# Optimization experiments

Hardware: AMD Instinct MI355X
Metric: run time of the kernel (lower is better)

The kernel has to match this reference:

```python
import jax, jax.numpy as jnp
import numpy as np

CLAMP = 1.0e6
LN_EPS = 1e-5
TWO_PI = 6.283185307179586


def _layernorm_last(x, gamma, beta):
    mu = jnp.mean(x, axis=-1, keepdims=True)
    var = jnp.var(x, axis=-1, keepdims=True)
    return (x - mu) * jax.lax.rsqrt(var + LN_EPS) * gamma + beta


def _candidates(xc):
    # xc: (C, B, S, D) pre-scaled + clamped input, one slice per candidate
    return jnp.stack([
        xc[0],
        xc[1] * xc[1],
        jnp.cos(TWO_PI * xc[2]),
        jnp.sin(xc[3]),
        jnp.exp(xc[4]),
        jnp.ones_like(xc[5]),
        xc[6] * xc[6] * xc[6],
        jnp.log(jnp.abs(xc[7]) + 1.0),
        jnp.sqrt(jnp.abs(xc[8])),
        jnp.tanh(xc[9]),
    ], axis=0)


def setup_inputs() -> dict:
    key = jax.random.key(0)
    ks = jax.random.split(key, 5)
    B, S, D, C = 4, 2048, 1024, 10
    return {
        "x": jax.random.normal(ks[0], (B, S, D), dtype=jnp.float32),
        "ln_gamma": jnp.ones((D,), dtype=jnp.float32),
        "ln_beta": jnp.zeros((D,), dtype=jnp.float32),
        "log_in_scale": jax.random.normal(ks[1], (C,), dtype=jnp.float32) * 0.05,
        "log_out_scale": jax.random.normal(ks[2], (C,), dtype=jnp.float32) * 0.05,
        "gate_w": jax.random.normal(ks[3], (C, D), dtype=jnp.float32) * (D ** -0.5),
        "gate_b": jnp.zeros((C,), dtype=jnp.float32),
    }


def reference(x, ln_gamma, ln_beta, log_in_scale, log_out_scale, gate_w, gate_b):
    # Input LayerNorm over D
    x_norm = _layernorm_last(x, ln_gamma, ln_beta)  # (B,S,D)

    in_s = jnp.exp(log_in_scale)    # (C,)
    out_s = jnp.exp(log_out_scale)  # (C,)

    # Per-candidate input scale + clamp
    xc = x_norm[None] * in_s[:, None, None, None]          # (C,B,S,D)
    xc = jnp.clip(xc, -CLAMP, CLAMP)

    cand = _candidates(xc) * out_s[:, None, None, None]    # (C,B,S,D)
    cand = jnp.clip(cand, -CLAMP, CLAMP)

    # permute to (B,S,C,D) and LayerNorm jointly over (C,D), no affine
    cand = jnp.transpose(cand, (1, 2, 0, 3))                # (B,S,C,D)
    mu = jnp.mean(cand, axis=(2, 3), keepdims=True)
    var = jnp.var(cand, axis=(2, 3), keepdims=True)
    cand = (cand - mu) * jax.lax.rsqrt(var + LN_EPS)
    cand = jnp.clip(cand, -CLAMP, CLAMP)
    cand = jnp.nan_to_num(cand, nan=0.0, posinf=CLAMP, neginf=-CLAMP)

    # Gate on the RAW input x (as in the torch code), softmax over candidates
    gate_logits = jnp.einsum('bsd,cd->bsc', x, gate_w) + gate_b  # (B,S,C)
    gate_weights = jax.nn.softmax(gate_logits, axis=-1)

    # Weighted sum over the candidate axis
    weighted = jnp.einsum('bsc,bscd->bsd', gate_weights, cand)   # (B,S,D)
    return weighted, gate_weights
```

## Files before the change

kernel.cpp:

```cpp
#include <hip/hip_runtime.h>
#include <math.h>

constexpr int D_DIM = 1024;
constexpr int C_DIM = 10;
constexpr int WPB   = 8;
constexpr int BLOCK = 64 * WPB;

constexpr float CLAMP_V  = 1.0e6f;
constexpr float LOG2E    = 1.4426950408889634f;
constexpr float LN2      = 0.6931471805599453f;
constexpr float INV_2PI  = 0.15915494309189535f;

__device__ __forceinline__ float2 pmul(float2 a, float2 b) {
    return make_float2(a.x * b.x, a.y * b.y);
}
__device__ __forceinline__ float2 pfma(float2 a, float2 b, float2 c) {
    return make_float2(fmaf(a.x, b.x, c.x), fmaf(a.y, b.y, c.y));
}
__device__ __forceinline__ float2 padd(float2 a, float2 b) {
    return make_float2(a.x + b.x, a.y + b.y);
}
__device__ __forceinline__ float2 bc(float s) { return make_float2(s, s); }

__device__ __forceinline__ float rfl(float x) {
    return __int_as_float(__builtin_amdgcn_readfirstlane(__float_as_int(x)));
}

template <int CTRL>
__device__ __forceinline__ float dpp_add(float v) {
    const int s = __builtin_amdgcn_update_dpp(
        0, __float_as_int(v), CTRL, 0xf, 0xf, false);
    return v + __int_as_float(s);
}
__device__ __forceinline__ float wave_sum_sgpr(float v) {
    v = dpp_add<0x111>(v);
    v = dpp_add<0x112>(v);
    v = dpp_add<0x114>(v);
    v = dpp_add<0x118>(v);
    v = dpp_add<0x142>(v);
    v = dpp_add<0x143>(v);
    return __int_as_float(__builtin_amdgcn_readlane(__float_as_int(v), 63));
}

__global__ __launch_bounds__(BLOCK)
void fused_sme_kernel(const float* __restrict__ x,
                      const float* __restrict__ ln_gamma,
                      const float* __restrict__ ln_beta,
                      const float* __restrict__ log_in_scale,
                      const float* __restrict__ log_out_scale,
                      const float* __restrict__ gate_w,
                      const float* __restrict__ gate_b,
                      float* __restrict__ out_weighted,
                      float* __restrict__ out_gate,
                      int tokens)
{
    const int t    = threadIdx.x;
    const int lane = t & 63;
    int token = blockIdx.x * WPB + (t >> 6);
    token = min(token, tokens - 1);

    __shared__ float gws[C_DIM * D_DIM];

    const float* xrow = x + (size_t)token * D_DIM;
    float4 xv[4];
#pragma unroll
    for (int k = 0; k < 4; ++k)
        xv[k] = *reinterpret_cast<const float4*>(xrow + k * 256 + (lane << 2));

#pragma unroll
    for (int i = 0; i < 5; ++i) {
        const int idx = t + i * BLOCK;
        reinterpret_cast<float4*>(gws)[idx] =
            reinterpret_cast<const float4*>(gate_w)[idx];
    }

    float r[12];
    {
        float2 s = bc(0.0f), q = bc(0.0f);
#pragma unroll
        for (int k = 0; k < 4; ++k) {
            const float2 lo = make_float2(xv[k].x, xv[k].y);
            const float2 hi = make_float2(xv[k].z, xv[k].w);
            s = padd(s, padd(lo, hi));
            q = pfma(lo, lo, q);
            q = pfma(hi, hi, q);
        }
        r[0] = wave_sum_sgpr(s.x + s.y);
        r[1] = wave_sum_sgpr(q.x + q.y);
    }

    __syncthreads();

#pragma unroll
    for (int c = 0; c < C_DIM; ++c) {
        const float* gr = gws + c * D_DIM + (lane << 2);
        float2 d2 = bc(0.0f);
#pragma unroll
        for (int k = 0; k < 4; ++k) {
            const float4 gw = *reinterpret_cast<const float4*>(gr + k * 256);
            d2 = pfma(make_float2(xv[k].x, xv[k].y), make_float2(gw.x, gw.y), d2);
            d2 = pfma(make_float2(xv[k].z, xv[k].w), make_float2(gw.z, gw.w), d2);
        }
        r[2 + c] = wave_sum_sgpr(d2.x + d2.y);
    }

    const float mu   = r[0] * (1.0f / D_DIM);
    const float var  = r[1] * (1.0f / D_DIM) - mu * mu;
    const float rstd = rfl(rsqrtf(var + 1e-5f));

    float w[C_DIM];
    float gmax = -3.4e38f;
#pragma unroll
    for (int c = 0; c < C_DIM; ++c) {
        w[c] = r[2 + c] + gate_b[c];
        gmax = fmaxf(gmax, w[c]);
    }
    float esum = 0.0f;
#pragma unroll
    for (int c = 0; c < C_DIM; ++c) {
        w[c] = __builtin_amdgcn_exp2f((w[c] - gmax) * LOG2E);
        esum += w[c];
    }
    const float rsum = __builtin_amdgcn_rcpf(esum);
#pragma unroll
    for (int c = 0; c < C_DIM; ++c) w[c] = rfl(w[c] * rsum);

    if (lane < C_DIM) out_gate[token * C_DIM + lane] = w[lane];

    float in_s[C_DIM], out_s[C_DIM];
#pragma unroll
    for (int c = 0; c < C_DIM; ++c) {
        in_s[c]  = __builtin_amdgcn_exp2f(log_in_scale[c]  * LOG2E);
        out_s[c] = __builtin_amdgcn_exp2f(log_out_scale[c] * LOG2E);
    }
    const float a0 = rfl(out_s[0] * in_s[0]);
    const float a1 = rfl(out_s[1] * in_s[1] * in_s[1]);
    const float k2 = rfl(in_s[2]),           o2 = rfl(out_s[2]);
    const float k3 = rfl(in_s[3] * INV_2PI), o3 = rfl(out_s[3]);
    const float k4 = rfl(in_s[4] * LOG2E),   o4 = rfl(out_s[4]);
    const float v5 = rfl(fminf(out_s[5], CLAMP_V));
    const float a6 = rfl(out_s[6] * in_s[6] * in_s[6] * in_s[6]);
    const float k7 = rfl(in_s[7]),           o7 = rfl(out_s[7] * LN2);
    const float k8 = rfl(in_s[8]),           o8 = rfl(out_s[8]);
    const float k9 = rfl(2.0f * in_s[9] * LOG2E);
    const float o9 = rfl(out_s[9]),          m9 = rfl(-2.0f * out_s[9]);

    float2 xn[8];
#pragma unroll
    for (int k = 0; k < 4; ++k) {
        const float4 gv = *reinterpret_cast<const float4*>(ln_gamma + k * 256 + (lane << 2));
        const float4 bv = *reinterpret_cast<const float4*>(ln_beta  + k * 256 + (lane << 2));
        const float2 zlo = pmul(padd(make_float2(xv[k].x, xv[k].y), bc(-mu)), bc(rstd));
        const float2 zhi = pmul(padd(make_float2(xv[k].z, xv[k].w), bc(-mu)), bc(rstd));
        xn[2 * k]     = pfma(zlo, make_float2(gv.x, gv.y), make_float2(bv.x, bv.y));
        xn[2 * k + 1] = pfma(zhi, make_float2(gv.z, gv.w), make_float2(bv.z, bv.w));
    }

    const float accbase = rfl(w[5] * v5);
    float2 S1 = bc(0.0f), S2 = bc(0.0f);

#pragma unroll
    for (int p = 0; p < 8; ++p) {
        const float2 xj = xn[p];
        const float2 ax = make_float2(fabsf(xj.x), fabsf(xj.y));
        const float2 x2 = pmul(xj, xj);

        const float2 v0 = pmul(bc(a0), xj);
        const float2 v1 = pmul(bc(a1), x2);

        float2 u2 = pmul(bc(k2), xj);
        u2 = padd(u2, make_float2(-rintf(u2.x), -rintf(u2.y)));
        const float2 v2 = pmul(bc(o2),
            make_float2(__builtin_amdgcn_cosf(u2.x), __builtin_amdgcn_cosf(u2.y)));

        float2 u3 = pmul(bc(k3), xj);
        u3 = padd(u3, make_float2(-rintf(u3.x), -rintf(u3.y)));
        const float2 v3 = pmul(bc(o3),
            make_float2(__builtin_amdgcn_sinf(u3.x), __builtin_amdgcn_sinf(u3.y)));

        const float2 u4 = pmul(bc(k4), xj);
        float2 v4 = pmul(bc(o4),
            make_float2(__builtin_amdgcn_exp2f(u4.x), __builtin_amdgcn_exp2f(u4.y)));
        v4 = make_float2(fminf(v4.x, CLAMP_V), fminf(v4.y, CLAMP_V));

        const float2 v6 = pmul(bc(a6), pmul(x2, xj));

        const float2 u7 = pfma(bc(k7), ax, bc(1.0f));
        const float2 v7 = pmul(bc(o7),
            make_float2(__builtin_amdgcn_logf(u7.x), __builtin_amdgcn_logf(u7.y)));

        const float2 u8 = pmul(bc(k8), ax);
        const float2 v8 = pmul(bc(o8),
            make_float2(__builtin_amdgcn_sqrtf(u8.x), __builtin_amdgcn_sqrtf(u8.y)));

        const float2 u9 = pmul(bc(k9), xj);
        const float2 e9 = padd(
            make_float2(__builtin_amdgcn_exp2f(u9.x), __builtin_amdgcn_exp2f(u9.y)),
            bc(1.0f));
        const float2 v9 = pfma(bc(m9),
            make_float2(__builtin_amdgcn_rcpf(e9.x), __builtin_amdgcn_rcpf(e9.y)),
            bc(o9));

        S1 = padd(S1, padd(padd(padd(v0, v1), padd(v2, v3)),
                           padd(padd(v4, v6), padd(padd(v7, v8), v9))));
        S2 = pfma(v0, v0, S2); S2 = pfma(v1, v1, S2); S2 = pfma(v2, v2, S2);
        S2 = pfma(v3, v3, S2); S2 = pfma(v4, v4, S2); S2 = pfma(v6, v6, S2);
        S2 = pfma(v7, v7, S2); S2 = pfma(v8, v8, S2); S2 = pfma(v9, v9, S2);

        float2 a = bc(accbase);
        a = pfma(bc(w[0]), v0, a); a = pfma(bc(w[1]), v1, a);
        a = pfma(bc(w[2]), v2, a); a = pfma(bc(w[3]), v3, a);
        a = pfma(bc(w[4]), v4, a); a = pfma(bc(w[6]), v6, a);
        a = pfma(bc(w[7]), v7, a); a = pfma(bc(w[8]), v8, a);
        a = pfma(bc(w[9]), v9, a);
        xn[p] = a;
    }

    const float s1 = wave_sum_sgpr(S1.x + S1.y + 16.0f * v5);
    const float s2 = wave_sum_sgpr(fmaf(16.0f * v5, v5, S2.x + S2.y));

    constexpr float rn = 1.0f / (float)(C_DIM * D_DIM);
    const float mu2  = s1 * rn;
    const float var2 = s2 * rn - mu2 * mu2;
    const float rsig = rfl(rsqrtf(var2 + 1e-5f));

    float* orow = out_weighted + (size_t)token * D_DIM;
#pragma unroll
    for (int k = 0; k < 4; ++k) {
        const float2 lo = pmul(padd(xn[2 * k],     bc(-mu2)), bc(rsig));
        const float2 hi = pmul(padd(xn[2 * k + 1], bc(-mu2)), bc(rsig));
        float4 o;
        o.x = lo.x; o.y = lo.y; o.z = hi.x; o.w = hi.y;
        *reinterpret_cast<float4*>(orow + k * 256 + (lane << 2)) = o;
    }
}

extern "C" void kernel_launch(void* const* d_in, const int* in_sizes, int n_in,
                              void* d_out, int out_size, void* d_ws, size_t ws_size,
                              hipStream_t stream) {
    const float* x   = (const float*)d_in[0];
    const float* lg  = (const float*)d_in[1];
    const float* lb  = (const float*)d_in[2];
    const float* lis = (const float*)d_in[3];
    const float* los = (const float*)d_in[4];
    const float* gw  = (const float*)d_in[5];
    const float* gb  = (const float*)d_in[6];

    const int tokens = in_sizes[0] / D_DIM;
    float* out      = (float*)d_out;
    float* out_gate = out + (size_t)tokens * D_DIM;

    const int grid = (tokens + WPB - 1) / WPB;
    hipLaunchKernelGGL(fused_sme_kernel, dim3(grid), dim3(BLOCK), 0, stream,
                       x, lg, lb, lis, los, gw, gb, out, out_gate, tokens);
}
```

Baseline: 29.76 us.

## Split each token across two waves and stage only nine gate rows in LDS

Each token is now handled by two wavefronts, each covering half of D, so a 512-thread block processes 4 tokens instead of 8. Partial sums for the LayerNorm statistics, gate logits and candidate statistics are combined through a small shared reduction array, which adds extra __syncthreads. Gate row 0 is read directly from global memory and only rows 1-9 are staged in LDS, making the LDS footprint smaller. The aim is more parallelism per token and less register pressure, at the cost of twice as many blocks, each of which reloads the gate weights, plus extra barriers.

```diff
diff --git a/kernel.cpp b/kernel.cpp
--- a/kernel.cpp
+++ b/kernel.cpp
@@ -3,8 +3,8 @@
 
 constexpr int D_DIM = 1024;
 constexpr int C_DIM = 10;
-constexpr int WPB   = 8;
-constexpr int BLOCK = 64 * WPB;
+constexpr int TPB   = 4;
+constexpr int BLOCK = 512;
 
 constexpr float CLAMP_V  = 1.0e6f;
 constexpr float LOG2E    = 1.4426950408889634f;
@@ -56,53 +56,75 @@
 {
     const int t    = threadIdx.x;
     const int lane = t & 63;
-    int token = blockIdx.x * WPB + (t >> 6);
+    const int h    = (t >> 6) & 1;
+    const int tl   = t >> 7;
+    int token = blockIdx.x * TPB + tl;
     token = min(token, tokens - 1);
 
-    __shared__ float gws[C_DIM * D_DIM];
-
-    const float* xrow = x + (size_t)token * D_DIM;
-    float4 xv[4];
-#pragma unroll
-    for (int k = 0; k < 4; ++k)
-        xv[k] = *reinterpret_cast<const float4*>(xrow + k * 256 + (lane << 2));
+    __shared__ float gws[9 * D_DIM];
+    __shared__ float red[TPB][2][14];
+
+    const int eoff = h * 512 + (lane << 2);
+    const float* xrow = x + (size_t)token * D_DIM + eoff;
+    float4 xv[2];
+#pragma unroll
+    for (int k = 0; k < 2; ++k)
+        xv[k] = *reinterpret_cast<const float4*>(xrow + k * 256);
 
 #pragma unroll
     for (int i = 0; i < 5; ++i) {
         const int idx = t + i * BLOCK;
-        reinterpret_cast<float4*>(gws)[idx] =
-            reinterpret_cast<const float4*>(gate_w)[idx];
+        if (idx < 9 * D_DIM / 4)
+            reinterpret_cast<float4*>(gws)[idx] =
+                reinterpret_cast<const float4*>(gate_w + D_DIM)[idx];
     }
 
     float r[12];
     {
-        float2 s = bc(0.0f), q = bc(0.0f);
-#pragma unroll
-        for (int k = 0; k < 4; ++k) {
+        float2 s = bc(0.0f), q = bc(0.0f), d0 = bc(0.0f);
+        const float* g0 = gate_w + eoff;
+#pragma unroll
+        for (int k = 0; k < 2; ++k) {
+            const float4 gv = *reinterpret_cast<const float4*>(g0 + k * 256);
             const float2 lo = make_float2(xv[k].x, xv[k].y);
             const float2 hi = make_float2(xv[k].z, xv[k].w);
             s = padd(s, padd(lo, hi));
             q = pfma(lo, lo, q);
             q = pfma(hi, hi, q);
+            d0 = pfma(lo, make_float2(gv.x, gv.y), d0);
+            d0 = pfma(hi, make_float2(gv.z, gv.w), d0);
         }
         r[0] = wave_sum_sgpr(s.x + s.y);
         r[1] = wave_sum_sgpr(q.x + q.y);
-    }
-
+        r[2] = wave_sum_sgpr(d0.x + d0.y);
+    }
+    if (lane == 0) {
+        red[tl][h][0] = r[0]; red[tl][h][1] = r[1]; red[tl][h][2] = r[2];
+    }
     __syncthreads();
-
-#pragma unroll
-    for (int c = 0; c < C_DIM; ++c) {
-        const float* gr = gws + c * D_DIM + (lane << 2);
+    r[0] += red[tl][h ^ 1][0];
+    r[1] += red[tl][h ^ 1][1];
+    r[2] += red[tl][h ^ 1][2];
+
+#pragma unroll
+    for (int c = 1; c < C_DIM; ++c) {
+        const float* gr = gws + (c - 1) * D_DIM + eoff;
         float2 d2 = bc(0.0f);
 #pragma unroll
-        for (int k = 0; k < 4; ++k) {
-            const float4 gw = *reinterpret_cast<const float4*>(gr + k * 256);
-            d2 = pfma(make_float2(xv[k].x, xv[k].y), make_float2(gw.x, gw.y), d2);
-            d2 = pfma(make_float2(xv[k].z, xv[k].w), make_float2(gw.z, gw.w), d2);
+        for (int k = 0; k < 2; ++k) {
+            const float4 gv = *reinterpret_cast<const float4*>(gr + k * 256);
+            d2 = pfma(make_float2(xv[k].x, xv[k].y), make_float2(gv.x, gv.y), d2);
+            d2 = pfma(make_float2(xv[k].z, xv[k].w), make_float2(gv.z, gv.w), d2);
         }
         r[2 + c] = wave_sum_sgpr(d2.x + d2.y);
     }
+    if (lane == 0) {
+#pragma unroll
+        for (int c = 1; c < C_DIM; ++c) red[tl][h][2 + c] = r[2 + c];
+    }
+    __syncthreads();
+#pragma unroll
+    for (int c = 1; c < C_DIM; ++c) r[2 + c] += red[tl][h ^ 1][2 + c];
 
     const float mu   = r[0] * (1.0f / D_DIM);
     const float var  = r[1] * (1.0f / D_DIM) - mu * mu;
@@ -125,7 +147,7 @@
 #pragma unroll
     for (int c = 0; c < C_DIM; ++c) w[c] = rfl(w[c] * rsum);
 
-    if (lane < C_DIM) out_gate[token * C_DIM + lane] = w[lane];
+    if (h == 0 && lane < C_DIM) out_gate[token * C_DIM + lane] = w[lane];
 
     float in_s[C_DIM], out_s[C_DIM];
 #pragma unroll
@@ -145,11 +167,11 @@
     const float k9 = rfl(2.0f * in_s[9] * LOG2E);
     const float o9 = rfl(out_s[9]),          m9 = rfl(-2.0f * out_s[9]);
 
-    float2 xn[8];
-#pragma unroll
-    for (int k = 0; k < 4; ++k) {
-        const float4 gv = *reinterpret_cast<const float4*>(ln_gamma + k * 256 + (lane << 2));
-        const float4 bv = *reinterpret_cast<const float4*>(ln_beta  + k * 256 + (lane << 2));
+    float2 xn[4];
+#pragma unroll
+    for (int k = 0; k < 2; ++k) {
+        const float4 gv = *reinterpret_cast<const float4*>(ln_gamma + eoff + k * 256);
+        const float4 bv = *reinterpret_cast<const float4*>(ln_beta  + eoff + k * 256);
         const float2 zlo = pmul(padd(make_float2(xv[k].x, xv[k].y), bc(-mu)), bc(rstd));
         const float2 zhi = pmul(padd(make_float2(xv[k].z, xv[k].w), bc(-mu)), bc(rstd));
         xn[2 * k]     = pfma(zlo, make_float2(gv.x, gv.y), make_float2(bv.x, bv.y));
@@ -160,7 +182,7 @@
     float2 S1 = bc(0.0f), S2 = bc(0.0f);
 
 #pragma unroll
-    for (int p = 0; p < 8; ++p) {
+    for (int p = 0; p < 4; ++p) {
         const float2 xj = xn[p];
         const float2 ax = make_float2(fabsf(xj.x), fabsf(xj.y));
         const float2 x2 = pmul(xj, xj);
@@ -216,22 +238,26 @@
         xn[p] = a;
     }
 
-    const float s1 = wave_sum_sgpr(S1.x + S1.y + 16.0f * v5);
-    const float s2 = wave_sum_sgpr(fmaf(16.0f * v5, v5, S2.x + S2.y));
+    float s1 = wave_sum_sgpr(S1.x + S1.y + 8.0f * v5);
+    float s2 = wave_sum_sgpr(fmaf(8.0f * v5, v5, S2.x + S2.y));
+    if (lane == 0) { red[tl][h][12] = s1; red[tl][h][13] = s2; }
+    __syncthreads();
+    s1 += red[tl][h ^ 1][12];
+    s2 += red[tl][h ^ 1][13];
 
     constexpr float rn = 1.0f / (float)(C_DIM * D_DIM);
     const float mu2  = s1 * rn;
     const float var2 = s2 * rn - mu2 * mu2;
     const float rsig = rfl(rsqrtf(var2 + 1e-5f));
 
-    float* orow = out_weighted + (size_t)token * D_DIM;
-#pragma unroll
-    for (int k = 0; k < 4; ++k) {
+    float* orow = out_weighted + (size_t)token * D_DIM + eoff;
+#pragma unroll
+    for (int k = 0; k < 2; ++k) {
         const float2 lo = pmul(padd(xn[2 * k],     bc(-mu2)), bc(rsig));
         const float2 hi = pmul(padd(xn[2 * k + 1], bc(-mu2)), bc(rsig));
         float4 o;
         o.x = lo.x; o.y = lo.y; o.z = hi.x; o.w = hi.y;
-        *reinterpret_cast<float4*>(orow + k * 256 + (lane << 2)) = o;
+        *reinterpret_cast<float4*>(orow + k * 256) = o;
     }
 }
 
@@ -250,7 +276,7 @@
     float* out      = (float*)d_out;
     float* out_gate = out + (size_t)tokens * D_DIM;
 
-    const int grid = (tokens + WPB - 1) / WPB;
+    const int grid = (tokens + TPB - 1) / TPB;
     hipLaunchKernelGGL(fused_sme_kernel, dim3(grid), dim3(BLOCK), 0, stream,
                        x, lg, lb, lis, los, gw, gb, out, out_gate, tokens);
 }
```

Measured after the change: 36.48 us. 1.23x slower.

## Split gate logits into separate MFMA kernel using split-bf16 emulation

Applied to the files above, without the earlier changes.

Moves the gate projection (x times gate_w) out of the fused kernel into its own kernel. That kernel computes 16-token tiles with bf16 MFMA instructions and uses a three-term hi/lo split to keep near-fp32 accuracy. The fused kernel then reads the logits from workspace, which drops the 40 KB shared-memory staging of gate_w per block and the ten per-token wave reductions. In exchange it adds a second launch, a second full read of x, and a workspace round-trip for the logits; block size also changes from 512 to 256 threads.

```diff
diff --git a/kernel.cpp b/kernel.cpp
--- a/kernel.cpp
+++ b/kernel.cpp
@@ -3,13 +3,14 @@
 
 constexpr int D_DIM = 1024;
 constexpr int C_DIM = 10;
-constexpr int WPB   = 8;
-constexpr int BLOCK = 64 * WPB;
 
 constexpr float CLAMP_V  = 1.0e6f;
 constexpr float LOG2E    = 1.4426950408889634f;
 constexpr float LN2      = 0.6931471805599453f;
 constexpr float INV_2PI  = 0.15915494309189535f;
+
+using bf16x8 = __attribute__((ext_vector_type(8))) short;
+using f32x4  = __attribute__((ext_vector_type(4))) float;
 
 __device__ __forceinline__ float2 pmul(float2 a, float2 b) {
     return make_float2(a.x * b.x, a.y * b.y);
@@ -42,77 +43,107 @@
     return __int_as_float(__builtin_amdgcn_readlane(__float_as_int(v), 63));
 }
 
-__global__ __launch_bounds__(BLOCK)
-void fused_sme_kernel(const float* __restrict__ x,
-                      const float* __restrict__ ln_gamma,
-                      const float* __restrict__ ln_beta,
-                      const float* __restrict__ log_in_scale,
-                      const float* __restrict__ log_out_scale,
-                      const float* __restrict__ gate_w,
-                      const float* __restrict__ gate_b,
-                      float* __restrict__ out_weighted,
-                      float* __restrict__ out_gate,
-                      int tokens)
+__global__ __launch_bounds__(64)
+void logits_kernel(const float* __restrict__ x,
+                   const float* __restrict__ gate_w,
+                   const float* __restrict__ gate_b,
+                   float* __restrict__ logits,
+                   int tokens)
 {
-    const int t    = threadIdx.x;
-    const int lane = t & 63;
-    int token = blockIdx.x * WPB + (t >> 6);
+    const int l    = threadIdx.x;
+    const int col  = l & 15;
+    const int kgrp = l >> 4;
+
+    const int tile = blockIdx.x;
+    const int arow = min(tile * 16 + col, tokens - 1);
+    const int wrow = (col < C_DIM) ? col : 0;
+    const float bm = (col < C_DIM) ? 1.0f : 0.0f;
+
+    const float* px = x + (size_t)arow * D_DIM + (kgrp << 3);
+    const float* pw = gate_w + (size_t)wrow * D_DIM + (kgrp << 3);
+
+    f32x4 acc0 = {0.f, 0.f, 0.f, 0.f};
+    f32x4 acc1 = {0.f, 0.f, 0.f, 0.f};
+    f32x4 acc2 = {0.f, 0.f, 0.f, 0.f};
+
+    for (int ks = 0; ks < D_DIM / 32; ++ks) {
+        const float4 a0 = *reinterpret_cast<const float4*>(px + ks * 32);
+        const float4 a1 = *reinterpret_cast<const float4*>(px + ks * 32 + 4);
+        const float4 b0 = *reinterpret_cast<const float4*>(pw + ks * 32);
+        const float4 b1 = *reinterpret_cast<const float4*>(pw + ks * 32 + 4);
+
+        const float af[8] = {a0.x, a0.y, a0.z, a0.w, a1.x, a1.y, a1.z, a1.w};
+        const float bf[8] = {b0.x * bm, b0.y * bm, b0.z * bm, b0.w * bm,
+                             b1.x * bm, b1.y * bm, b1.z * bm, b1.w * bm};
+        bf16x8 ah, al, bh, bl;
+#pragma unroll
+        for (int j = 0; j < 8; ++j) {
+            const unsigned ua = __float_as_uint(af[j]);
+            ah[j] = (short)(ua >> 16);
+            al[j] = (short)(__float_as_uint(
+                        af[j] - __uint_as_float(ua & 0xffff0000u)) >> 16);
+            const unsigned ub = __float_as_uint(bf[j]);
+            bh[j] = (short)(ub >> 16);
+            bl[j] = (short)(__float_as_uint(
+                        bf[j] - __uint_as_float(ub & 0xffff0000u)) >> 16);
+        }
+        acc0 = __builtin_amdgcn_mfma_f32_16x16x32_bf16(ah, bh, acc0, 0, 0, 0);
+        acc1 = __builtin_amdgcn_mfma_f32_16x16x32_bf16(ah, bl, acc1, 0, 0, 0);
+        acc2 = __builtin_amdgcn_mfma_f32_16x16x32_bf16(al, bh, acc2, 0, 0, 0);
+    }
+
+    const float bias = (col < C_DIM) ? gate_b[col] : 0.0f;
+#pragma unroll
+    for (int r = 0; r < 4; ++r) {
+        const int trow = tile * 16 + (l >> 4) * 4 + r;
+        if (trow < tokens)
+            logits[trow * 16 + col] = (acc0[r] + acc1[r]) + acc2[r] + bias;
+    }
+}
+
+__global__ __launch_bounds__(256)
+void fused_kernel(const float* __restrict__ x,
+                  const float* __restrict__ ln_gamma,
+                  const float* __restrict__ ln_beta,
+                  const float* __restrict__ log_in_scale,
+                  const float* __restrict__ log_out_scale,
+                  const float* __restrict__ logits,
+                  float* __restrict__ out_weighted,
+                  float* __restrict__ out_gate,
+                  int tokens)
+{
+    const int lane = threadIdx.x & 63;
+    int token = blockIdx.x * 4 + (threadIdx.x >> 6);
     token = min(token, tokens - 1);
 
-    __shared__ float gws[C_DIM * D_DIM];
-
-    const float* xrow = x + (size_t)token * D_DIM;
+    const float* xrow = x + (size_t)token * D_DIM + (lane << 2);
     float4 xv[4];
 #pragma unroll
     for (int k = 0; k < 4; ++k)
-        xv[k] = *reinterpret_cast<const float4*>(xrow + k * 256 + (lane << 2));
-
-#pragma unroll
-    for (int i = 0; i < 5; ++i) {
-        const int idx = t + i * BLOCK;
-        reinterpret_cast<float4*>(gws)[idx] =
-            reinterpret_cast<const float4*>(gate_w)[idx];
-    }
-
-    float r[12];
-    {
-        float2 s = bc(0.0f), q = bc(0.0f);
-#pragma unroll
-        for (int k = 0; k < 4; ++k) {
-            const float2 lo = make_float2(xv[k].x, xv[k].y);
-            const float2 hi = make_float2(xv[k].z, xv[k].w);
-            s = padd(s, padd(lo, hi));
-            q = pfma(lo, lo, q);
-            q = pfma(hi, hi, q);
-        }
-        r[0] = wave_sum_sgpr(s.x + s.y);
-        r[1] = wave_sum_sgpr(q.x + q.y);
-    }
-
-    __syncthreads();
-
-#pragma unroll
-    for (int c = 0; c < C_DIM; ++c) {
-        const float* gr = gws + c * D_DIM + (lane << 2);
-        float2 d2 = bc(0.0f);
-#pragma unroll
-        for (int k = 0; k < 4; ++k) {
-            const float4 gw = *reinterpret_cast<const float4*>(gr + k * 256);
-            d2 = pfma(make_float2(xv[k].x, xv[k].y), make_float2(gw.x, gw.y), d2);
-            d2 = pfma(make_float2(xv[k].z, xv[k].w), make_float2(gw.z, gw.w), d2);
-        }
-        r[2 + c] = wave_sum_sgpr(d2.x + d2.y);
-    }
-
-    const float mu   = r[0] * (1.0f / D_DIM);
-    const float var  = r[1] * (1.0f / D_DIM) - mu * mu;
+        xv[k] = *reinterpret_cast<const float4*>(xrow + k * 256);
+
+    float2 s = bc(0.0f), q = bc(0.0f);
+#pragma unroll
+    for (int k = 0; k < 4; ++k) {
+        const float2 lo = make_float2(xv[k].x, xv[k].y);
+        const float2 hi = make_float2(xv[k].z, xv[k].w);
+        s = padd(s, padd(lo, hi));
+        q = pfma(lo, lo, q);
+        q = pfma(hi, hi, q);
+    }
+    const float r0 = wave_sum_sgpr(s.x + s.y);
+    const float r1 = wave_sum_sgpr(q.x + q.y);
+
+    const float mu   = r0 * (1.0f / D_DIM);
+    const float var  = r1 * (1.0f / D_DIM) - mu * mu;
     const float rstd = rfl(rsqrtf(var + 1e-5f));
 
+    const float* st = logits + token * 16;
     float w[C_DIM];
     float gmax = -3.4e38f;
 #pragma unroll
     for (int c = 0; c < C_DIM; ++c) {
-        w[c] = r[2 + c] + gate_b[c];
+        w[c] = st[c];
         gmax = fmaxf(gmax, w[c]);
     }
     float esum = 0.0f;
@@ -224,14 +255,14 @@
     const float var2 = s2 * rn - mu2 * mu2;
     const float rsig = rfl(rsqrtf(var2 + 1e-5f));
 
-    float* orow = out_weighted + (size_t)token * D_DIM;
+    float* orow = out_weighted + (size_t)token * D_DIM + (lane << 2);
 #pragma unroll
     for (int k = 0; k < 4; ++k) {
         const float2 lo = pmul(padd(xn[2 * k],     bc(-mu2)), bc(rsig));
         const float2 hi = pmul(padd(xn[2 * k + 1], bc(-mu2)), bc(rsig));
         float4 o;
         o.x = lo.x; o.y = lo.y; o.z = hi.x; o.w = hi.y;
-        *reinterpret_cast<float4*>(orow + k * 256 + (lane << 2)) = o;
+        *reinterpret_cast<float4*>(orow + k * 256) = o;
     }
 }
 
@@ -249,8 +280,13 @@
     const int tokens = in_sizes[0] / D_DIM;
     float* out      = (float*)d_out;
     float* out_gate = out + (size_t)tokens * D_DIM;
-
-    const int grid = (tokens + WPB - 1) / WPB;
-    hipLaunchKernelGGL(fused_sme_kernel, dim3(grid), dim3(BLOCK), 0, stream,
-                       x, lg, lb, lis, los, gw, gb, out, out_gate, tokens);
-}
+    float* logits   = (float*)d_ws;
+
+    const int tiles = (tokens + 15) / 16;
+    hipLaunchKernelGGL(logits_kernel, dim3(tiles), dim3(64), 0, stream,
+                       x, gw, gb, logits, tokens);
+
+    const int g2 = (tokens + 3) / 4;
+    hipLaunchKernelGGL(fused_kernel, dim3(g2), dim3(256), 0, stream,
+                       x, lg, lb, lis, los, logits, out, out_gate, tokens);
+}
```

Result: slower. 41.32 us (+38.9%).
